# Optimization experiments

Measured on AMD Instinct MI355X. Metric: run time of the kernel, lower is better.

The kernel has to match this reference:

```python
import jax, jax.numpy as jnp
import numpy as np

B, N, D = 64, 100, 32            # batch, nodes, node feature size
FE = [96, 160, 192]              # edge-MLP layer sizes
FN = [256, 256, 32]              # node-MLP layer sizes
ALPHA = 0.2                      # leaky relu slope


def _lin_init(key, fan_in, fan_out):
    kw, kb = jax.random.split(key)
    bound = 1.0 / np.sqrt(fan_in)
    w = jax.random.uniform(kw, (fan_in, fan_out), jnp.float32, -bound, bound)
    b = jax.random.uniform(kb, (fan_out,), jnp.float32, -bound, bound)
    return w, b


def setup_inputs() -> dict:
    key = jax.random.key(0)
    ks = jax.random.split(key, 7)
    d = {"x": jax.random.normal(ks[0], (B, N, D), jnp.float32)}
    fe_sizes = [2 * D] + FE                    # edge MLP: in = concat(x_i, x_j)
    fn_sizes = [FE[-1] + D] + FN               # node MLP: in = concat(agg, x)
    for li in range(3):
        w, b = _lin_init(ks[1 + li], fe_sizes[li], fe_sizes[li + 1])
        d[f"fe_w{li}"], d[f"fe_b{li}"] = w, b
    for li in range(3):
        w, b = _lin_init(ks[4 + li], fn_sizes[li], fn_sizes[li + 1])
        d[f"fn_w{li}"], d[f"fn_b{li}"] = w, b
    return d


def reference(x, fe_w0, fe_b0, fe_w1, fe_b1, fe_w2, fe_b2,
              fn_w0, fn_b0, fn_w1, fn_b1, fn_w2, fn_b2):
    b, n, d = x.shape
    lr = lambda v: jax.nn.leaky_relu(v, ALPHA)
    # fully-connected pairwise edge features: A[b,i,j] = concat(x_i, x_j)
    xi = jnp.broadcast_to(x[:, :, None, :], (b, n, n, d))
    xj = jnp.broadcast_to(x[:, None, :, :], (b, n, n, d))
    a = jnp.concatenate([xi, xj], axis=-1)          # [b, n, n, 2d]
    # edge MLP (fe): leaky relu after every layer (final_linear=False)
    a = lr(a @ fe_w0 + fe_b0)
    a = lr(a @ fe_w1 + fe_b1)
    a = lr(a @ fe_w2 + fe_b2)                       # [b, n, n, FE[-1]]
    # sum aggregation over neighbors j
    agg = jnp.sum(a, axis=2)                        # [b, n, FE[-1]]
    # node MLP (fn): final layer linear (final_linear=True)
    h = jnp.concatenate([agg, x], axis=-1)          # [b, n, FE[-1]+d]
    h = lr(h @ fn_w0 + fn_b0)
    h = lr(h @ fn_w1 + fn_b1)
    h = h @ fn_w2 + fn_b2                           # [b, n, FN[-1]]
    return h
```

## Files before the change

### kernel.cpp

```cpp
#include <hip/hip_runtime.h>

#define B_    64
#define N_    100
#define D_    32
#define F0    96
#define F1    160
#define F2    192
#define HID   256
#define FOUT  32

typedef unsigned short u16;
typedef unsigned int   u32;
typedef u16   u16x8 __attribute__((ext_vector_type(8)));
typedef __bf16 bf16x8 __attribute__((ext_vector_type(8)));
typedef float  fx4   __attribute__((ext_vector_type(4)));

__device__ __forceinline__ u16 f2bfu(float f) {
    u32 u = __float_as_uint(f);
    u += 0x7fffu + ((u >> 16) & 1u);
    return (u16)(u >> 16);
}
__device__ __forceinline__ float lrelu(float v) { return v > 0.f ? v : 0.2f * v; }

__device__ __forceinline__ bf16x8 fragLds(const u16* p) {
    return __builtin_bit_cast(bf16x8, *(const u16x8*)p);
}
__device__ __forceinline__ bf16x8 fragGbl(const u16* __restrict__ p) {
    return __builtin_bit_cast(bf16x8, *(const u16x8*)p);
}
#define MFMA(a, b, c) __builtin_amdgcn_mfma_f32_16x16x32_bf16((a), (b), (c), 0, 0, 0)

#define OFF_P     0u
#define OFF_V     2457600u
#define OFF_AGG   4915200u
#define OFF_PACK  7372800u
#define PK_W1     0
#define PK_W2     15360
#define PK_N0     46080
#define PK_N1     103424
#define PK_N2     168960
#define PK_TOTAL  177152

#define PV_BLOCKS 2400
#define PACK_BLOCKS 346

__global__ __launch_bounds__(512) void prep_kernel(
    const float* __restrict__ x,
    const float* __restrict__ few0, const float* __restrict__ feb0,
    const float* __restrict__ few1, const float* __restrict__ few2,
    const float* __restrict__ fnw0, const float* __restrict__ fnw1,
    const float* __restrict__ fnw2,
    float* __restrict__ P, float* __restrict__ V, u16* __restrict__ wpack)
{
    const int blk = blockIdx.x, tid = threadIdx.x;
    if (blk < PV_BLOCKS) {
        int o = blk * 512 + tid;
        int r = o / 192, h = o - r * 192;
        const float* xr = x + r * D_;
        if (h < F0) {
            float acc = feb0[h];
            #pragma unroll
            for (int d = 0; d < D_; ++d) acc = fmaf(xr[d], few0[d * F0 + h], acc);
            P[r * F0 + h] = acc;
        } else {
            int k = h - F0;
            float acc = 0.f;
            #pragma unroll
            for (int d = 0; d < D_; ++d) acc = fmaf(xr[d], few0[(D_ + d) * F0 + k], acc);
            V[r * F0 + k] = acc;
        }
    } else {
        int p = (blk - PV_BLOCKS) * 512 + tid;
        const float* src; int start, Ncols, NT;
        if (p < PK_W2)      { start = PK_W1; src = few1; Ncols = F1;   NT = 10; }
        else if (p < PK_N0) { start = PK_W2; src = few2; Ncols = F2;   NT = 12; }
        else if (p < PK_N1) { start = PK_N0; src = fnw0; Ncols = HID;  NT = 16; }
        else if (p < PK_N2) { start = PK_N1; src = fnw1; Ncols = HID;  NT = 16; }
        else                { start = PK_N2; src = fnw2; Ncols = FOUT; NT = 2;  }
        int local = p - start;
        int j = local & 7, lane = (local >> 3) & 63, rest = local >> 9;
        int nt = rest % NT, kt = rest / NT;
        int n = 16 * nt + (lane & 15);
        int k = 32 * kt + 8 * (lane >> 4) + j;
        wpack[p] = f2bfu(src[k * Ncols + n]);
    }
}

__global__ __launch_bounds__(512, 4) void edge_kernel(
    const float* __restrict__ P, const float* __restrict__ V,
    const u16* __restrict__ W1p, const u16* __restrict__ W2p,
    const float* __restrict__ feb1, const float* __restrict__ feb2,
    u16* __restrict__ agg)
{
    const int i = blockIdx.x, b = blockIdx.y;
    const int tid = threadIdx.x, ld = tid & 63, wv = tid >> 6;
    const int wn = wv & 3, wm = wv >> 2;
    const int row = b * N_ + i;

    __shared__ __align__(16) u16  sA0p[7 * 3 * 512];
    __shared__ __align__(16) u16  sA1p[7 * 5 * 512];
    __shared__ __align__(16) float sP[F0];
    __shared__ __align__(16) float sAggP[2 * F2];

    if (tid < F0) sP[tid] = P[row * F0 + tid];
    __syncthreads();

    {
        const float* Vb = V + b * N_ * F0;
        #pragma unroll
        for (int s = 0; s < 21; ++s) {
            int e = tid + 512 * s;
            int j = e & 7, lane = (e >> 3) & 63, rest = e >> 9;
            int kt = rest % 3, mt = rest / 3;
            int k = 32 * kt + 8 * (lane >> 4) + j;
            int m = 16 * mt + (lane & 15);
            float v = 0.f;
            if (m < N_) v = lrelu(sP[k] + Vb[m * F0 + k]);
            sA0p[e] = f2bfu(v);
        }
    }
    __syncthreads();

    const int mtB = wm ? 4 : 0, mtE = wm ? 7 : 4;
    const int c = ld & 15, rlo = (ld >> 4) * 4;

    {
        const int nCnt = (wn < 2) ? 3 : 2;
        bf16x8 bw[3][3]; float bias[3];
        #pragma unroll
        for (int t = 0; t < 3; ++t) if (t < nCnt) {
            int nt = wn + 4 * t;
            bias[t] = feb1[16 * nt + c];
            #pragma unroll
            for (int kt = 0; kt < 3; ++kt)
                bw[t][kt] = fragGbl(W1p + (size_t)((kt * 10 + nt) * 64 + ld) * 8);
        }
        for (int mt = mtB; mt < mtE; ++mt) {
            bf16x8 a[3];
            #pragma unroll
            for (int kt = 0; kt < 3; ++kt)
                a[kt] = fragLds(sA0p + ((mt * 3 + kt) * 64 + ld) * 8);
            fx4 acc[3];
            #pragma unroll
            for (int t = 0; t < 3; ++t) acc[t] = (fx4){0.f, 0.f, 0.f, 0.f};
            #pragma unroll
            for (int kt = 0; kt < 3; ++kt)
                #pragma unroll
                for (int t = 0; t < 3; ++t)
                    if (t < nCnt) acc[t] = MFMA(a[kt], bw[t][kt], acc[t]);
            #pragma unroll
            for (int t = 0; t < 3; ++t) if (t < nCnt) {
                int f = 16 * (wn + 4 * t) + c;
                int kt2 = f >> 5, lq = (f >> 3) & 3, j2 = f & 7;
                #pragma unroll
                for (int r = 0; r < 4; ++r) {
                    float val = lrelu(acc[t][r] + bias[t]);
                    int lane2 = (rlo + r) + 16 * lq;
                    sA1p[((mt * 5 + kt2) * 64 + lane2) * 8 + j2] = f2bfu(val);
                }
            }
        }
    }
    __syncthreads();

    {
        bf16x8 bw[3][5]; float bias[3];
        float aggp[3] = {0.f, 0.f, 0.f};
        #pragma unroll
        for (int t = 0; t < 3; ++t) {
            int nt = wn + 4 * t;
            bias[t] = feb2[16 * nt + c];
            #pragma unroll
            for (int kt = 0; kt < 5; ++kt)
                bw[t][kt] = fragGbl(W2p + (size_t)((kt * 12 + nt) * 64 + ld) * 8);
        }
        for (int mt = mtB; mt < mtE; ++mt) {
            bf16x8 a[5];
            #pragma unroll
            for (int kt = 0; kt < 5; ++kt)
                a[kt] = fragLds(sA1p + ((mt * 5 + kt) * 64 + ld) * 8);
            fx4 acc[3];
            #pragma unroll
            for (int t = 0; t < 3; ++t) acc[t] = (fx4){0.f, 0.f, 0.f, 0.f};
            #pragma unroll
            for (int kt = 0; kt < 5; ++kt)
                #pragma unroll
                for (int t = 0; t < 3; ++t)
                    acc[t] = MFMA(a[kt], bw[t][kt], acc[t]);
            bool ok = (mt < 6) || (rlo == 0);
            if (ok) {
                #pragma unroll
                for (int t = 0; t < 3; ++t)
                    #pragma unroll
                    for (int r = 0; r < 4; ++r)
                        aggp[t] += lrelu(acc[t][r] + bias[t]);
            }
        }
        #pragma unroll
        for (int t = 0; t < 3; ++t) {
            aggp[t] += __shfl_xor(aggp[t], 16, 64);
            aggp[t] += __shfl_xor(aggp[t], 32, 64);
        }
        if (ld < 16) {
            #pragma unroll
            for (int t = 0; t < 3; ++t)
                sAggP[wm * F2 + 16 * (wn + 4 * t) + ld] = aggp[t];
        }
    }
    __syncthreads();

    if (tid < F2) {
        float v = sAggP[tid] + sAggP[F2 + tid];
        agg[(size_t)row * F2 + tid] = f2bfu(v);
    }
}

__global__ __launch_bounds__(512, 4) void node_kernel(
    const u16* __restrict__ agg, const float* __restrict__ x,
    const u16* __restrict__ n0p, const u16* __restrict__ n1p,
    const u16* __restrict__ n2p,
    const float* __restrict__ fnb0, const float* __restrict__ fnb1,
    const float* __restrict__ fnb2,
    float* __restrict__ out)
{
    const int blk = blockIdx.x;
    const int tid = threadIdx.x, ld = tid & 63, wv = tid >> 6;
    const int wn = wv & 3, mt = wv >> 2;
    const int c = ld & 15, rlo = (ld >> 4) * 4;

    __shared__ __align__(16) u16 sH0p[2 * 7 * 512];
    __shared__ __align__(16) u16 sH1p[2 * 8 * 512];
    __shared__ __align__(16) u16 sH2p[2 * 8 * 512];

    #pragma unroll
    for (int s = 0; s < 14; ++s) {
        int e = tid + 512 * s;
        int j = e & 7, lane = (e >> 3) & 63, rest = e >> 9;
        int kt = rest % 7, mtt = rest / 7;
        int k = 32 * kt + 8 * (lane >> 4) + j;
        int m = 16 * mtt + (lane & 15);
        int g = 32 * blk + m;
        u16 val = (k < F2) ? agg[(size_t)g * F2 + k]
                           : f2bfu(x[(size_t)g * D_ + (k - F2)]);
        sH0p[e] = val;
    }
    __syncthreads();

    {
        fx4 acc[4];
        #pragma unroll
        for (int t = 0; t < 4; ++t) acc[t] = (fx4){0.f, 0.f, 0.f, 0.f};
        for (int kt = 0; kt < 7; ++kt) {
            bf16x8 a = fragLds(sH0p + ((mt * 7 + kt) * 64 + ld) * 8);
            #pragma unroll
            for (int t = 0; t < 4; ++t) {
                bf16x8 bw = fragGbl(n0p + (size_t)((kt * 16 + wn + 4 * t) * 64 + ld) * 8);
                acc[t] = MFMA(a, bw, acc[t]);
            }
        }
        #pragma unroll
        for (int t = 0; t < 4; ++t) {
            int f = 16 * (wn + 4 * t) + c;
            float bias = fnb0[f];
            int kt2 = f >> 5, lq = (f >> 3) & 3, j2 = f & 7;
            #pragma unroll
            for (int r = 0; r < 4; ++r) {
                float val = lrelu(acc[t][r] + bias);
                sH1p[((mt * 8 + kt2) * 64 + (rlo + r) + 16 * lq) * 8 + j2] = f2bfu(val);
            }
        }
    }
    __syncthreads();

    {
        fx4 acc[4];
        #pragma unroll
        for (int t = 0; t < 4; ++t) acc[t] = (fx4){0.f, 0.f, 0.f, 0.f};
        for (int kt = 0; kt < 8; ++kt) {
            bf16x8 a = fragLds(sH1p + ((mt * 8 + kt) * 64 + ld) * 8);
            #pragma unroll
            for (int t = 0; t < 4; ++t) {
                bf16x8 bw = fragGbl(n1p + (size_t)((kt * 16 + wn + 4 * t) * 64 + ld) * 8);
                acc[t] = MFMA(a, bw, acc[t]);
            }
        }
        #pragma unroll
        for (int t = 0; t < 4; ++t) {
            int f = 16 * (wn + 4 * t) + c;
            float bias = fnb1[f];
            int kt2 = f >> 5, lq = (f >> 3) & 3, j2 = f & 7;
            #pragma unroll
            for (int r = 0; r < 4; ++r) {
                float val = lrelu(acc[t][r] + bias);
                sH2p[((mt * 8 + kt2) * 64 + (rlo + r) + 16 * lq) * 8 + j2] = f2bfu(val);
            }
        }
    }
    __syncthreads();

    if (wv < 4) {
        int mt2 = wv >> 1, nt = wv & 1;
        fx4 acc = (fx4){0.f, 0.f, 0.f, 0.f};
        for (int kt = 0; kt < 8; ++kt) {
            bf16x8 a = fragLds(sH2p + ((mt2 * 8 + kt) * 64 + ld) * 8);
            bf16x8 bw = fragGbl(n2p + (size_t)((kt * 2 + nt) * 64 + ld) * 8);
            acc = MFMA(a, bw, acc);
        }
        int f = 16 * nt + c;
        float bias = fnb2[f];
        #pragma unroll
        for (int r = 0; r < 4; ++r) {
            int g = 32 * blk + 16 * mt2 + rlo + r;
            out[(size_t)g * FOUT + f] = acc[r] + bias;
        }
    }
}

extern "C" void kernel_launch(void* const* d_in, const int* in_sizes, int n_in,
                              void* d_out, int out_size, void* d_ws, size_t ws_size,
                              hipStream_t stream) {
    const float* x    = (const float*)d_in[0];
    const float* few0 = (const float*)d_in[1];
    const float* feb0 = (const float*)d_in[2];
    const float* few1 = (const float*)d_in[3];
    const float* feb1 = (const float*)d_in[4];
    const float* few2 = (const float*)d_in[5];
    const float* feb2 = (const float*)d_in[6];
    const float* fnw0 = (const float*)d_in[7];
    const float* fnb0 = (const float*)d_in[8];
    const float* fnw1 = (const float*)d_in[9];
    const float* fnb1 = (const float*)d_in[10];
    const float* fnw2 = (const float*)d_in[11];
    const float* fnb2 = (const float*)d_in[12];

    char* w = (char*)d_ws;
    float* P    = (float*)(w + OFF_P);
    float* V    = (float*)(w + OFF_V);
    u16*   agg  = (u16*)(w + OFF_AGG);
    u16*   pack = (u16*)(w + OFF_PACK);

    prep_kernel<<<PV_BLOCKS + PACK_BLOCKS, 512, 0, stream>>>(
        x, few0, feb0, few1, few2, fnw0, fnw1, fnw2, P, V, pack);

    edge_kernel<<<dim3(N_, B_), 512, 0, stream>>>(
        P, V, pack + PK_W1, pack + PK_W2, feb1, feb2, agg);

    node_kernel<<<200, 512, 0, stream>>>(
        agg, x, pack + PK_N0, pack + PK_N1, pack + PK_N2,
        fnb0, fnb1, fnb2, (float*)d_out);
}
```

Baseline: 209.2 us.

## Restructure edge and node kernels with swapped MFMA operands and vectorized packing

The edge kernel now treats weights as the MFMA A operand and activations as B, so each wave owns a set of output feature tiles across several row tiles. Layer-1 weights are preloaded into registers before the first barrier, and layer-2 weights are streamed in K slabs. The A0 build uses float4 loads and packed bf16 conversion, and leaky-relu becomes a branchless fmax. The node kernel processes 16 rows per block with twice as many blocks and vectorized input staging. These changes aim to cut LDS traffic, conversion overhead and launch imbalance, at the cost of more accumulator registers and a different reduction pattern.

```diff
diff --git a/kernel.cpp b/kernel.cpp
--- a/kernel.cpp
+++ b/kernel.cpp
@@ -13,6 +13,7 @@
 typedef unsigned int   u32;
 typedef u16   u16x8 __attribute__((ext_vector_type(8)));
 typedef __bf16 bf16x8 __attribute__((ext_vector_type(8)));
+typedef __bf16 bf16x2 __attribute__((ext_vector_type(2)));
 typedef float  fx4   __attribute__((ext_vector_type(4)));
 
 __device__ __forceinline__ u16 f2bfu(float f) {
@@ -20,7 +21,17 @@
     u += 0x7fffu + ((u >> 16) & 1u);
     return (u16)(u >> 16);
 }
-__device__ __forceinline__ float lrelu(float v) { return v > 0.f ? v : 0.2f * v; }
+#if __has_builtin(__builtin_amdgcn_cvt_pk_bf16_f32)
+__device__ __forceinline__ u32 pk2(float a, float b) {
+    bf16x2 t = __builtin_amdgcn_cvt_pk_bf16_f32(a, b);
+    return __builtin_bit_cast(u32, t);
+}
+#else
+__device__ __forceinline__ u32 pk2(float a, float b) {
+    return (u32)f2bfu(a) | ((u32)f2bfu(b) << 16);
+}
+#endif
+__device__ __forceinline__ float lrelu(float v) { return fmaxf(v, 0.2f * v); }
 
 __device__ __forceinline__ bf16x8 fragLds(const u16* p) {
     return __builtin_bit_cast(bf16x8, *(const u16x8*)p);
@@ -94,125 +105,161 @@
 {
     const int i = blockIdx.x, b = blockIdx.y;
     const int tid = threadIdx.x, ld = tid & 63, wv = tid >> 6;
-    const int wn = wv & 3, wm = wv >> 2;
+    const int c = ld & 15, Q = ld >> 4;
     const int row = b * N_ + i;
 
-    __shared__ __align__(16) u16  sA0p[7 * 3 * 512];
-    __shared__ __align__(16) u16  sA1p[7 * 5 * 512];
+    __shared__ __align__(16) u16  sB0[3 * 7 * 64 * 8];
+    __shared__ __align__(16) u16  sB1[5 * 7 * 64 * 8];
     __shared__ __align__(16) float sP[F0];
     __shared__ __align__(16) float sAggP[2 * F2];
 
-    if (tid < F0) sP[tid] = P[row * F0 + tid];
+    if (tid < 24) ((float4*)sP)[tid] = ((const float4*)(P + (size_t)row * F0))[tid];
+
+    const int wf = wv >> 2;
+    const int wm = wv & 3;
+    const int ftb = wf * 5;
+    bf16x8 aw1[5][3];
+    #pragma unroll
+    for (int t = 0; t < 5; ++t)
+        #pragma unroll
+        for (int kt = 0; kt < 3; ++kt)
+            aw1[t][kt] = fragGbl(W1p + (size_t)((kt * 10 + ftb + t) * 64 + ld) * 8);
+
     __syncthreads();
 
     {
-        const float* Vb = V + b * N_ * F0;
-        #pragma unroll
-        for (int s = 0; s < 21; ++s) {
-            int e = tid + 512 * s;
-            int j = e & 7, lane = (e >> 3) & 63, rest = e >> 9;
-            int kt = rest % 3, mt = rest / 3;
-            int k = 32 * kt + 8 * (lane >> 4) + j;
-            int m = 16 * mt + (lane & 15);
-            float v = 0.f;
-            if (m < N_) v = lrelu(sP[k] + Vb[m * F0 + k]);
-            sA0p[e] = f2bfu(v);
-        }
-    }
-    __syncthreads();
-
-    const int mtB = wm ? 4 : 0, mtE = wm ? 7 : 4;
-    const int c = ld & 15, rlo = (ld >> 4) * 4;
+        const float* Vb = V + (size_t)b * (N_ * F0);
+        #pragma unroll
+        for (int s = 0; s < 3; ++s) {
+            int o = tid + 512 * s;
+            if (o < 1344) {
+                int mt = o / 192;
+                int rem = o - mt * 192;
+                int kt = rem >> 6, lane = rem & 63;
+                int m = 16 * mt + (lane & 15);
+                int kb = 32 * kt + 8 * (lane >> 4);
+                const float* vp = Vb + m * F0 + kb;
+                float4 va = *(const float4*)vp;
+                float4 vb = *(const float4*)(vp + 4);
+                float4 pa = *(const float4*)&sP[kb];
+                float4 pb = *(const float4*)&sP[kb + 4];
+                uint4 w;
+                w.x = pk2(lrelu(pa.x + va.x), lrelu(pa.y + va.y));
+                w.y = pk2(lrelu(pa.z + va.z), lrelu(pa.w + va.w));
+                w.z = pk2(lrelu(pb.x + vb.x), lrelu(pb.y + vb.y));
+                w.w = pk2(lrelu(pb.z + vb.z), lrelu(pb.w + vb.w));
+                *(uint4*)&sB0[o * 8] = w;
+            }
+        }
+    }
+    __syncthreads();
 
     {
-        const int nCnt = (wn < 2) ? 3 : 2;
-        bf16x8 bw[3][3]; float bias[3];
-        #pragma unroll
-        for (int t = 0; t < 3; ++t) if (t < nCnt) {
-            int nt = wn + 4 * t;
-            bias[t] = feb1[16 * nt + c];
+        const int nmi = (wm == 3) ? 1 : 2;
+        for (int mi = 0; mi < nmi; ++mi) {
+            int mt = wm + 4 * mi;
+            bf16x8 b0[3];
             #pragma unroll
             for (int kt = 0; kt < 3; ++kt)
-                bw[t][kt] = fragGbl(W1p + (size_t)((kt * 10 + nt) * 64 + ld) * 8);
-        }
-        for (int mt = mtB; mt < mtE; ++mt) {
-            bf16x8 a[3];
-            #pragma unroll
-            for (int kt = 0; kt < 3; ++kt)
-                a[kt] = fragLds(sA0p + ((mt * 3 + kt) * 64 + ld) * 8);
-            fx4 acc[3];
-            #pragma unroll
-            for (int t = 0; t < 3; ++t) acc[t] = (fx4){0.f, 0.f, 0.f, 0.f};
+                b0[kt] = fragLds(sB0 + ((mt * 3 + kt) * 64 + ld) * 8);
+            fx4 acc[5];
+            #pragma unroll
+            for (int t = 0; t < 5; ++t) acc[t] = (fx4){0.f, 0.f, 0.f, 0.f};
             #pragma unroll
             for (int kt = 0; kt < 3; ++kt)
                 #pragma unroll
-                for (int t = 0; t < 3; ++t)
-                    if (t < nCnt) acc[t] = MFMA(a[kt], bw[t][kt], acc[t]);
-            #pragma unroll
-            for (int t = 0; t < 3; ++t) if (t < nCnt) {
-                int f = 16 * (wn + 4 * t) + c;
-                int kt2 = f >> 5, lq = (f >> 3) & 3, j2 = f & 7;
+                for (int t = 0; t < 5; ++t)
+                    acc[t] = MFMA(aw1[t][kt], b0[kt], acc[t]);
+            #pragma unroll
+            for (int t = 0; t < 5; ++t) {
+                int f0 = 16 * (ftb + t) + 4 * Q;
+                float4 bias = *(const float4*)(feb1 + f0);
+                u32 lo = pk2(lrelu(acc[t][0] + bias.x), lrelu(acc[t][1] + bias.y));
+                u32 hi = pk2(lrelu(acc[t][2] + bias.z), lrelu(acc[t][3] + bias.w));
+                int kt2 = f0 >> 5, o8 = (f0 >> 3) & 3, j0 = f0 & 7;
+                int lane2 = c + 16 * o8;
+                *(uint2*)&sB1[((mt * 5 + kt2) * 64 + lane2) * 8 + j0] = (uint2){lo, hi};
+            }
+        }
+    }
+    __syncthreads();
+
+    {
+        const int wf2 = wv >> 1;
+        const int wm2 = wv & 1;
+        const int nmi = 4 - wm2;
+        fx4 acc[4][3];
+        #pragma unroll
+        for (int mi = 0; mi < 4; ++mi)
+            #pragma unroll
+            for (int t = 0; t < 3; ++t) acc[mi][t] = (fx4){0.f, 0.f, 0.f, 0.f};
+
+        #pragma unroll
+        for (int slab = 0; slab < 3; ++slab) {
+            const int k0 = slab * 2, nk = (slab == 2) ? 1 : 2;
+            bf16x8 aw2[3][2];
+            #pragma unroll
+            for (int t = 0; t < 3; ++t)
+                #pragma unroll
+                for (int kk = 0; kk < 2; ++kk)
+                    if (kk < nk)
+                        aw2[t][kk] = fragGbl(W2p + (size_t)(((k0 + kk) * 12 + wf2 + 4 * t) * 64 + ld) * 8);
+            for (int mi = 0; mi < nmi; ++mi) {
+                int mt = wm2 + 2 * mi;
+                #pragma unroll
+                for (int kk = 0; kk < 2; ++kk) {
+                    if (kk < nk) {
+                        bf16x8 b1 = fragLds(sB1 + ((mt * 5 + k0 + kk) * 64 + ld) * 8);
+                        #pragma unroll
+                        for (int t = 0; t < 3; ++t)
+                            acc[mi][t] = MFMA(aw2[t][kk], b1, acc[mi][t]);
+                    }
+                }
+            }
+        }
+        float ag[3][4];
+        #pragma unroll
+        for (int t = 0; t < 3; ++t)
+            #pragma unroll
+            for (int r = 0; r < 4; ++r) ag[t][r] = 0.f;
+        #pragma unroll
+        for (int t = 0; t < 3; ++t) {
+            int f0 = 16 * (wf2 + 4 * t) + 4 * Q;
+            float4 bias = *(const float4*)(feb2 + f0);
+            for (int mi = 0; mi < nmi; ++mi) {
+                int mt = wm2 + 2 * mi;
                 #pragma unroll
                 for (int r = 0; r < 4; ++r) {
-                    float val = lrelu(acc[t][r] + bias[t]);
-                    int lane2 = (rlo + r) + 16 * lq;
-                    sA1p[((mt * 5 + kt2) * 64 + lane2) * 8 + j2] = f2bfu(val);
+                    float bb = (r == 0) ? bias.x : (r == 1) ? bias.y : (r == 2) ? bias.z : bias.w;
+                    float val = lrelu(acc[mi][t][r] + bb);
+                    if (mt == 6 && c >= 4) val = 0.f;
+                    ag[t][r] += val;
                 }
             }
         }
-    }
-    __syncthreads();
-
-    {
-        bf16x8 bw[3][5]; float bias[3];
-        float aggp[3] = {0.f, 0.f, 0.f};
-        #pragma unroll
-        for (int t = 0; t < 3; ++t) {
-            int nt = wn + 4 * t;
-            bias[t] = feb2[16 * nt + c];
-            #pragma unroll
-            for (int kt = 0; kt < 5; ++kt)
-                bw[t][kt] = fragGbl(W2p + (size_t)((kt * 12 + nt) * 64 + ld) * 8);
-        }
-        for (int mt = mtB; mt < mtE; ++mt) {
-            bf16x8 a[5];
-            #pragma unroll
-            for (int kt = 0; kt < 5; ++kt)
-                a[kt] = fragLds(sA1p + ((mt * 5 + kt) * 64 + ld) * 8);
-            fx4 acc[3];
-            #pragma unroll
-            for (int t = 0; t < 3; ++t) acc[t] = (fx4){0.f, 0.f, 0.f, 0.f};
-            #pragma unroll
-            for (int kt = 0; kt < 5; ++kt)
+        #pragma unroll
+        for (int t = 0; t < 3; ++t)
+            #pragma unroll
+            for (int r = 0; r < 4; ++r) {
+                float v = ag[t][r];
+                v += __shfl_xor(v, 1);
+                v += __shfl_xor(v, 2);
+                v += __shfl_xor(v, 4);
+                v += __shfl_xor(v, 8);
+                ag[t][r] = v;
+            }
+        if (c == 0) {
+            #pragma unroll
+            for (int t = 0; t < 3; ++t)
                 #pragma unroll
-                for (int t = 0; t < 3; ++t)
-                    acc[t] = MFMA(a[kt], bw[t][kt], acc[t]);
-            bool ok = (mt < 6) || (rlo == 0);
-            if (ok) {
-                #pragma unroll
-                for (int t = 0; t < 3; ++t)
-                    #pragma unroll
-                    for (int r = 0; r < 4; ++r)
-                        aggp[t] += lrelu(acc[t][r] + bias[t]);
-            }
-        }
-        #pragma unroll
-        for (int t = 0; t < 3; ++t) {
-            aggp[t] += __shfl_xor(aggp[t], 16, 64);
-            aggp[t] += __shfl_xor(aggp[t], 32, 64);
-        }
-        if (ld < 16) {
-            #pragma unroll
-            for (int t = 0; t < 3; ++t)
-                sAggP[wm * F2 + 16 * (wn + 4 * t) + ld] = aggp[t];
-        }
-    }
-    __syncthreads();
-
-    if (tid < F2) {
-        float v = sAggP[tid] + sAggP[F2 + tid];
-        agg[(size_t)row * F2 + tid] = f2bfu(v);
-    }
+                for (int r = 0; r < 4; ++r)
+                    sAggP[wm2 * F2 + 16 * (wf2 + 4 * t) + 4 * Q + r] = ag[t][r];
+        }
+    }
+    __syncthreads();
+
+    if (tid < F2)
+        agg[(size_t)row * F2 + tid] = f2bfu(sAggP[tid] + sAggP[F2 + tid]);
 }
 
 __global__ __launch_bounds__(512, 4) void node_kernel(
@@ -225,84 +272,88 @@
 {
     const int blk = blockIdx.x;
     const int tid = threadIdx.x, ld = tid & 63, wv = tid >> 6;
-    const int wn = wv & 3, mt = wv >> 2;
-    const int c = ld & 15, rlo = (ld >> 4) * 4;
-
-    __shared__ __align__(16) u16 sH0p[2 * 7 * 512];
-    __shared__ __align__(16) u16 sH1p[2 * 8 * 512];
-    __shared__ __align__(16) u16 sH2p[2 * 8 * 512];
-
-    #pragma unroll
-    for (int s = 0; s < 14; ++s) {
-        int e = tid + 512 * s;
-        int j = e & 7, lane = (e >> 3) & 63, rest = e >> 9;
-        int kt = rest % 7, mtt = rest / 7;
-        int k = 32 * kt + 8 * (lane >> 4) + j;
-        int m = 16 * mtt + (lane & 15);
-        int g = 32 * blk + m;
-        u16 val = (k < F2) ? agg[(size_t)g * F2 + k]
-                           : f2bfu(x[(size_t)g * D_ + (k - F2)]);
-        sH0p[e] = val;
+    const int c = ld & 15, Q = ld >> 4;
+
+    __shared__ __align__(16) u16 sH0p[7 * 512];
+    __shared__ __align__(16) u16 sH1p[8 * 512];
+    __shared__ __align__(16) u16 sH2p[8 * 512];
+
+    if (tid < 448) {
+        int kt = tid >> 6, lane = tid & 63;
+        int m = lane & 15;
+        int kb = 32 * kt + 8 * (lane >> 4);
+        int g = 16 * blk + m;
+        uint4 w;
+        if (kb < F2) {
+            w = *(const uint4*)(agg + (size_t)g * F2 + kb);
+        } else {
+            const float* xp = x + (size_t)g * D_ + (kb - F2);
+            float4 a = *(const float4*)xp;
+            float4 bb = *(const float4*)(xp + 4);
+            w.x = pk2(a.x, a.y);  w.y = pk2(a.z, a.w);
+            w.z = pk2(bb.x, bb.y); w.w = pk2(bb.z, bb.w);
+        }
+        *(uint4*)&sH0p[tid * 8] = w;
     }
     __syncthreads();
 
     {
-        fx4 acc[4];
-        #pragma unroll
-        for (int t = 0; t < 4; ++t) acc[t] = (fx4){0.f, 0.f, 0.f, 0.f};
+        fx4 acc[2];
+        #pragma unroll
+        for (int t = 0; t < 2; ++t) acc[t] = (fx4){0.f, 0.f, 0.f, 0.f};
         for (int kt = 0; kt < 7; ++kt) {
-            bf16x8 a = fragLds(sH0p + ((mt * 7 + kt) * 64 + ld) * 8);
-            #pragma unroll
-            for (int t = 0; t < 4; ++t) {
-                bf16x8 bw = fragGbl(n0p + (size_t)((kt * 16 + wn + 4 * t) * 64 + ld) * 8);
+            bf16x8 a = fragLds(sH0p + (kt * 64 + ld) * 8);
+            #pragma unroll
+            for (int t = 0; t < 2; ++t) {
+                bf16x8 bw = fragGbl(n0p + (size_t)((kt * 16 + wv + 8 * t) * 64 + ld) * 8);
                 acc[t] = MFMA(a, bw, acc[t]);
             }
         }
         #pragma unroll
-        for (int t = 0; t < 4; ++t) {
-            int f = 16 * (wn + 4 * t) + c;
+        for (int t = 0; t < 2; ++t) {
+            int f = 16 * (wv + 8 * t) + c;
             float bias = fnb0[f];
-            int kt2 = f >> 5, lq = (f >> 3) & 3, j2 = f & 7;
+            int kt2 = f >> 5, o8 = (f >> 3) & 3, j2 = f & 7;
             #pragma unroll
             for (int r = 0; r < 4; ++r) {
                 float val = lrelu(acc[t][r] + bias);
-                sH1p[((mt * 8 + kt2) * 64 + (rlo + r) + 16 * lq) * 8 + j2] = f2bfu(val);
+                sH1p[((kt2) * 64 + (4 * Q + r) + 16 * o8) * 8 + j2] = f2bfu(val);
             }
         }
     }
     __syncthreads();
 
     {
-        fx4 acc[4];
-        #pragma unroll
-        for (int t = 0; t < 4; ++t) acc[t] = (fx4){0.f, 0.f, 0.f, 0.f};
+        fx4 acc[2];
+        #pragma unroll
+        for (int t = 0; t < 2; ++t) acc[t] = (fx4){0.f, 0.f, 0.f, 0.f};
         for (int kt = 0; kt < 8; ++kt) {
-            bf16x8 a = fragLds(sH1p + ((mt * 8 + kt) * 64 + ld) * 8);
-            #pragma unroll
-            for (int t = 0; t < 4; ++t) {
-                bf16x8 bw = fragGbl(n1p + (size_t)((kt * 16 + wn + 4 * t) * 64 + ld) * 8);
+            bf16x8 a = fragLds(sH1p + (kt * 64 + ld) * 8);
+            #pragma unroll
+            for (int t = 0; t < 2; ++t) {
+                bf16x8 bw = fragGbl(n1p + (size_t)((kt * 16 + wv + 8 * t) * 64 + ld) * 8);
                 acc[t] = MFMA(a, bw, acc[t]);
             }
         }
         #pragma unroll
-        for (int t = 0; t < 4; ++t) {
-            int f = 16 * (wn + 4 * t) + c;
+        for (int t = 0; t < 2; ++t) {
+            int f = 16 * (wv + 8 * t) + c;
             float bias = fnb1[f];
-            int kt2 = f >> 5, lq = (f >> 3) & 3, j2 = f & 7;
+            int kt2 = f >> 5, o8 = (f >> 3) & 3, j2 = f & 7;
             #pragma unroll
             for (int r = 0; r < 4; ++r) {
                 float val = lrelu(acc[t][r] + bias);
-                sH2p[((mt * 8 + kt2) * 64 + (rlo + r) + 16 * lq) * 8 + j2] = f2bfu(val);
-            }
-        }
-    }
-    __syncthreads();
-
-    if (wv < 4) {
-        int mt2 = wv >> 1, nt = wv & 1;
+                sH2p[((kt2) * 64 + (4 * Q + r) + 16 * o8) * 8 + j2] = f2bfu(val);
+            }
+        }
+    }
+    __syncthreads();
+
+    if (wv < 2) {
+        int nt = wv;
         fx4 acc = (fx4){0.f, 0.f, 0.f, 0.f};
         for (int kt = 0; kt < 8; ++kt) {
-            bf16x8 a = fragLds(sH2p + ((mt2 * 8 + kt) * 64 + ld) * 8);
+            bf16x8 a = fragLds(sH2p + (kt * 64 + ld) * 8);
             bf16x8 bw = fragGbl(n2p + (size_t)((kt * 2 + nt) * 64 + ld) * 8);
             acc = MFMA(a, bw, acc);
         }
@@ -310,7 +361,7 @@
         float bias = fnb2[f];
         #pragma unroll
         for (int r = 0; r < 4; ++r) {
-            int g = 32 * blk + 16 * mt2 + rlo + r;
+            int g = 16 * blk + 4 * Q + r;
             out[(size_t)g * FOUT + f] = acc[r] + bias;
         }
     }
@@ -345,7 +396,7 @@
     edge_kernel<<<dim3(N_, B_), 512, 0, stream>>>(
         P, V, pack + PK_W1, pack + PK_W2, feb1, feb2, agg);
 
-    node_kernel<<<200, 512, 0, stream>>>(
+    node_kernel<<<400, 512, 0, stream>>>(
         agg, x, pack + PK_N0, pack + PK_N1, pack + PK_N2,
         fnb0, fnb1, fnb2, (float*)d_out);
 }
```

New measurement: 680.3 us. 225% more time.
